# Performance work log

Hardware: AMD Instinct MI355X
Metric: run time of the kernel (lower is better)

## Reference

```python
import jax, jax.numpy as jnp
import numpy as np

B = 4096
NUM_FEATURES = 2048
NUM_NEURONS = 1024
NUM_TARGETS = 8
NNZ1 = 65536
NNZ2 = 8192


def _sparse_linear(x, w, b, rows, cols, n_out):
    """y[b, o] = sum_{e: rows[e]==o} w[e] * x[b, cols[e]] + b[o].

    x: [B, n_in], w: [nnz], rows/cols: [nnz] int, b: [n_out].
    """
    prod = x[:, cols] * w  # [B, nnz] gather + elementwise
    # segment_sum reduces over leading axis -> work on [nnz, B]
    y = jax.ops.segment_sum(prod.T, rows, num_segments=n_out)  # [n_out, B]
    return y.T + b


def setup_inputs() -> dict:
    key = jax.random.key(0)
    ks = jax.random.split(key, 9)
    x = jax.random.normal(ks[0], (B, NUM_FEATURES), dtype=jnp.float32)
    w1 = jax.random.normal(ks[1], (NNZ1,), dtype=jnp.float32) * 0.05
    b1 = jax.random.normal(ks[2], (NUM_NEURONS,), dtype=jnp.float32) * 0.05
    w2 = jax.random.normal(ks[3], (NNZ2,), dtype=jnp.float32) * 0.05
    b2 = jax.random.normal(ks[4], (NUM_TARGETS,), dtype=jnp.float32) * 0.05
    conn1_out = jax.random.randint(ks[5], (NNZ1,), 0, NUM_NEURONS, dtype=jnp.int64 if jax.config.jax_enable_x64 else jnp.int32)
    conn1_in = jax.random.randint(ks[6], (NNZ1,), 0, NUM_FEATURES, dtype=conn1_out.dtype)
    conn2_out = jax.random.randint(ks[7], (NNZ2,), 0, NUM_TARGETS, dtype=conn1_out.dtype)
    conn2_in = jax.random.randint(ks[8], (NNZ2,), 0, NUM_NEURONS, dtype=conn1_out.dtype)
    return {
        "x": x, "w1": w1, "b1": b1, "w2": w2, "b2": b2,
        "conn1_out": conn1_out, "conn1_in": conn1_in,
        "conn2_out": conn2_out, "conn2_in": conn2_in,
    }


def reference(x, w1, b1, w2, b2, conn1_out, conn1_in, conn2_out, conn2_in):
    h = jax.nn.sigmoid(_sparse_linear(x, w1, b1, conn1_out, conn1_in, b1.shape[0]))
    out = _sparse_linear(h, w2, b2, conn2_out, conn2_in, b2.shape[0])
    # num_targets = 8 != 1, so no final sigmoid (matches CrossEntropyLoss path)
    return out
```

## Files before the change

### kernel.cpp

```cpp
#include <hip/hip_runtime.h>
#include <math.h>

#define BATCH 4096
#define NFEAT 2048
#define NNEUR 1024
#define NTGT  8
#define NNZ1  65536
#define NNZ2  8192

#define BM 128
#define BN 64
#define BK 64
#define KSTEPS (NFEAT / BK)

typedef short  bf16x8 __attribute__((ext_vector_type(8)));
typedef float  f32x4  __attribute__((ext_vector_type(4)));

#define OFF_W1F  ((size_t)0)
#define OFF_W2D  ((size_t)8388608)
#define OFF_W1B  ((size_t)8421376)

#define ZERO_FLOAT4 526336
#define OUT_FLOAT4  (BATCH * NTGT / 4)

__device__ __forceinline__ unsigned short f2bf(float f) {
    union { float f; unsigned int u; } a; a.f = f;
    unsigned int u = a.u;
    u += 0x7fffu + ((u >> 16) & 1u);
    return (unsigned short)(u >> 16);
}

__device__ __forceinline__ uint4 pk8(float4 lo, float4 hi) {
    uint4 r;
    asm("v_cvt_pk_bf16_f32 %0, %1, %2" : "=v"(r.x) : "v"(lo.x), "v"(lo.y));
    asm("v_cvt_pk_bf16_f32 %0, %1, %2" : "=v"(r.y) : "v"(lo.z), "v"(lo.w));
    asm("v_cvt_pk_bf16_f32 %0, %1, %2" : "=v"(r.z) : "v"(hi.x), "v"(hi.y));
    asm("v_cvt_pk_bf16_f32 %0, %1, %2" : "=v"(r.w) : "v"(hi.z), "v"(hi.w));
    return r;
}

__global__ void k_zero(float4* __restrict__ ws4, float4* __restrict__ out4,
                       const float* __restrict__ b2) {
    int i = blockIdx.x * blockDim.x + threadIdx.x;
    if (i < ZERO_FLOAT4) {
        ws4[i] = make_float4(0.f, 0.f, 0.f, 0.f);
    } else {
        int j = i - ZERO_FLOAT4;
        if (j < OUT_FLOAT4) {
            int p = (j & 1) * 4;
            out4[j] = make_float4(b2[p], b2[p + 1], b2[p + 2], b2[p + 3]);
        }
    }
}

__global__ void k_build(const float* __restrict__ w1, const int* __restrict__ c1o,
                        const int* __restrict__ c1i,
                        const float* __restrict__ w2, const int* __restrict__ c2o,
                        const int* __restrict__ c2i,
                        float* __restrict__ W1f, float* __restrict__ W2d) {
    int i = blockIdx.x * blockDim.x + threadIdx.x;
    if (i < NNZ1) {
        atomicAdd(&W1f[(size_t)c1o[i] * NFEAT + c1i[i]], w1[i]);
    } else {
        int j = i - NNZ1;
        if (j < NNZ2) atomicAdd(&W2d[c2i[j] * NTGT + c2o[j]], w2[j]);
    }
}

__global__ void k_convert(const float* __restrict__ W1f, unsigned short* __restrict__ W1b) {
    int i = blockIdx.x * blockDim.x + threadIdx.x;
    float4 v = ((const float4*)W1f)[i];
    ushort4 o;
    o.x = f2bf(v.x); o.y = f2bf(v.y); o.z = f2bf(v.z); o.w = f2bf(v.w);
    ((ushort4*)W1b)[i] = o;
}

__global__ __launch_bounds__(256) void k_gemm(const unsigned short* __restrict__ W1b,
                                              const float* __restrict__ x,
                                              const float* __restrict__ b1,
                                              const float* __restrict__ W2d,
                                              float* __restrict__ out) {
    __shared__ unsigned short ldsA[2][BM * BK];
    __shared__ unsigned short ldsB[2][BN * BK];
    __shared__ float s_w2[BM][NTGT];
    __shared__ float s_b1[BM];
    __shared__ float s_pt[2][BN][NTGT];

    int bid = blockIdx.x;
    int v   = bid >> 3;
    int n0  = ((bid & 7) * 8 + (v >> 3)) * BN;
    int mt  = v & 7;
    int m0  = mt * BM;

    int tid  = threadIdx.x;
    int wv   = tid >> 6;
    int lane = tid & 63;
    int wm = wv >> 1, wn = wv & 1;
    int lr = lane & 15, lg = lane >> 4;

    for (int i = tid; i < BM * NTGT; i += 256)
        s_w2[i >> 3][i & 7] = W2d[(m0 + (i >> 3)) * NTGT + (i & 7)];
    if (tid < BM) s_b1[tid] = b1[m0 + tid];

    f32x4 zero4 = {0.f, 0.f, 0.f, 0.f};
    f32x4 acc[4][2];
#pragma unroll
    for (int i = 0; i < 4; ++i)
#pragma unroll
        for (int j = 0; j < 2; ++j) acc[i][j] = zero4;

    int r0 = tid >> 3, s0 = tid & 7;
    const unsigned short* gA0 = &W1b[(size_t)(m0 + r0) * NFEAT + s0 * 8];
    const unsigned short* gA1 = gA0 + 32 * NFEAT;
    const unsigned short* gA2 = gA0 + 64 * NFEAT;
    const unsigned short* gA3 = gA0 + 96 * NFEAT;
    const float* gB0 = &x[(size_t)(n0 + r0) * NFEAT + s0 * 8];
    const float* gB1 = gB0 + 32 * NFEAT;
    const int iw0 = r0 * 8 + (s0 ^ (r0 & 7));
    const int iw1 = iw0 + 256, iw2 = iw0 + 512, iw3 = iw0 + 768;

    bf16x8 A0a, A0b, A0c, A0d;  float4 B0a, B0b, B0c, B0d;
    bf16x8 A1a, A1b, A1c, A1d;  float4 B1a, B1b, B1c, B1d;
    bf16x8 af0[4], af1[4], bg0[2], bg1[2];

#define LOADS0(T) do { int kk = (T) * BK;                           \
        A0a = *(const bf16x8*)(gA0 + kk); A0b = *(const bf16x8*)(gA1 + kk); \
        A0c = *(const bf16x8*)(gA2 + kk); A0d = *(const bf16x8*)(gA3 + kk); \
        B0a = *(const float4*)(gB0 + kk); B0b = *(const float4*)(gB0 + kk + 4); \
        B0c = *(const float4*)(gB1 + kk); B0d = *(const float4*)(gB1 + kk + 4); } while (0)
#define LOADS1(T) do { int kk = (T) * BK;                           \
        A1a = *(const bf16x8*)(gA0 + kk); A1b = *(const bf16x8*)(gA1 + kk); \
        A1c = *(const bf16x8*)(gA2 + kk); A1d = *(const bf16x8*)(gA3 + kk); \
        B1a = *(const float4*)(gB0 + kk); B1b = *(const float4*)(gB0 + kk + 4); \
        B1c = *(const float4*)(gB1 + kk); B1d = *(const float4*)(gB1 + kk + 4); } while (0)

#define STORE0(BUF) do {                                            \
        bf16x8* dA = (bf16x8*)&ldsA[BUF][0];                        \
        dA[iw0] = A0a; dA[iw1] = A0b; dA[iw2] = A0c; dA[iw3] = A0d; \
        uint4* dB = (uint4*)&ldsB[BUF][0];                          \
        dB[iw0] = pk8(B0a, B0b); dB[iw1] = pk8(B0c, B0d); } while (0)
#define STORE1(BUF) do {                                            \
        bf16x8* dA = (bf16x8*)&ldsA[BUF][0];                        \
        dA[iw0] = A1a; dA[iw1] = A1b; dA[iw2] = A1c; dA[iw3] = A1d; \
        uint4* dB = (uint4*)&ldsB[BUF][0];                          \
        dB[iw0] = pk8(B1a, B1b); dB[iw1] = pk8(B1c, B1d); } while (0)

#define READF(BUF) do {                                             \
        const unsigned short* bA = ldsA[BUF];                       \
        const unsigned short* bB = ldsB[BUF];                       \
        _Pragma("unroll")                                           \
        for (int i = 0; i < 4; ++i) {                               \
            int rowa = wm * 64 + i * 16 + lr;                       \
            af0[i] = *(const bf16x8*)&bA[(rowa * 8 + ((lg)     ^ (rowa & 7))) * 8]; \
            af1[i] = *(const bf16x8*)&bA[(rowa * 8 + ((4 + lg) ^ (rowa & 7))) * 8]; \
        }                                                           \
        _Pragma("unroll")                                           \
        for (int j = 0; j < 2; ++j) {                               \
            int rowb = wn * 32 + j * 16 + lr;                       \
            bg0[j] = *(const bf16x8*)&bB[(rowb * 8 + ((lg)     ^ (rowb & 7))) * 8]; \
            bg1[j] = *(const bf16x8*)&bB[(rowb * 8 + ((4 + lg) ^ (rowb & 7))) * 8]; \
        }                                                           \
    } while (0)

#define MFMAS() do {                                                \
        _Pragma("unroll")                                           \
        for (int i = 0; i < 4; ++i)                                 \
            _Pragma("unroll")                                       \
            for (int j = 0; j < 2; ++j)                             \
                acc[i][j] = __builtin_amdgcn_mfma_f32_16x16x32_bf16(af0[i], bg0[j], acc[i][j], 0, 0, 0); \
        _Pragma("unroll")                                           \
        for (int i = 0; i < 4; ++i)                                 \
            _Pragma("unroll")                                       \
            for (int j = 0; j < 2; ++j)                             \
                acc[i][j] = __builtin_amdgcn_mfma_f32_16x16x32_bf16(af1[i], bg1[j], acc[i][j], 0, 0, 0); \
    } while (0)

#define LDSFENCE() asm volatile("s_waitcnt lgkmcnt(0)" ::: "memory")

    LOADS0(0);
    LOADS1(1);
    STORE0(0);
    LDSFENCE();
    __builtin_amdgcn_s_barrier();

#pragma unroll 1
    for (int p = 0; p < 15; ++p) {
        int e = 2 * p;
        LOADS0(e + 2);
        STORE1(1);
        READF(0);
        MFMAS();
        LDSFENCE();
        __builtin_amdgcn_s_barrier();
        LOADS1(e + 3);
        STORE0(0);
        READF(1);
        MFMAS();
        LDSFENCE();
        __builtin_amdgcn_s_barrier();
    }
    STORE1(1);
    READF(0);
    MFMAS();
    LDSFENCE();
    __builtin_amdgcn_s_barrier();
    READF(1);
    MFMAS();

#undef LOADS0
#undef LOADS1
#undef STORE0
#undef STORE1
#undef READF
#undef MFMAS
#undef LDSFENCE

    float pt[2][NTGT];
#pragma unroll
    for (int j = 0; j < 2; ++j)
#pragma unroll
        for (int t = 0; t < NTGT; ++t) pt[j][t] = 0.f;

#pragma unroll
    for (int i = 0; i < 4; ++i) {
#pragma unroll
        for (int r = 0; r < 4; ++r) {
            int ml = wm * 64 + i * 16 + lg * 4 + r;
            float bn = s_b1[ml];
#pragma unroll
            for (int j = 0; j < 2; ++j) {
                float h = 1.f / (1.f + __expf(-(acc[i][j][r] + bn)));
#pragma unroll
                for (int t = 0; t < NTGT; ++t)
                    pt[j][t] += h * s_w2[ml][t];
            }
        }
    }
#pragma unroll
    for (int j = 0; j < 2; ++j)
#pragma unroll
        for (int t = 0; t < NTGT; ++t) {
            float val = pt[j][t];
            val += __shfl_xor(val, 16, 64);
            val += __shfl_xor(val, 32, 64);
            pt[j][t] = val;
        }
    if (lg == 0) {
#pragma unroll
        for (int j = 0; j < 2; ++j) {
            int nl = wn * 32 + j * 16 + lr;
#pragma unroll
            for (int t = 0; t < NTGT; ++t)
                s_pt[wm][nl][t] = pt[j][t];
        }
    }
    __syncthreads();
    for (int idx = tid; idx < BN * NTGT; idx += 256) {
        int nl = idx >> 3, t = idx & 7;
        atomicAdd(&out[(size_t)(n0 + nl) * NTGT + t], s_pt[0][nl][t] + s_pt[1][nl][t]);
    }
}

extern "C" void kernel_launch(void* const* d_in, const int* in_sizes, int n_in,
                              void* d_out, int out_size, void* d_ws, size_t ws_size,
                              hipStream_t stream) {
    (void)in_sizes; (void)n_in; (void)out_size; (void)ws_size;
    const float* x   = (const float*)d_in[0];
    const float* w1  = (const float*)d_in[1];
    const float* b1  = (const float*)d_in[2];
    const float* w2  = (const float*)d_in[3];
    const float* b2  = (const float*)d_in[4];
    const int*   c1o = (const int*)d_in[5];
    const int*   c1i = (const int*)d_in[6];
    const int*   c2o = (const int*)d_in[7];
    const int*   c2i = (const int*)d_in[8];
    float* out = (float*)d_out;

    char* ws = (char*)d_ws;
    float*          W1f  = (float*)(ws + OFF_W1F);
    float*          W2d  = (float*)(ws + OFF_W2D);
    unsigned short* W1b  = (unsigned short*)(ws + OFF_W1B);

    k_zero<<<(ZERO_FLOAT4 + OUT_FLOAT4 + 255) / 256, 256, 0, stream>>>(
        (float4*)ws, (float4*)out, b2);

    k_build<<<(NNZ1 + NNZ2) / 256, 256, 0, stream>>>(w1, c1o, c1i, w2, c2o, c2i, W1f, W2d);

    k_convert<<<NNEUR * NFEAT / 4 / 256, 256, 0, stream>>>(W1f, W1b);

    k_gemm<<<(NNEUR / BM) * (BATCH / BN), 256, 0, stream>>>(W1b, x, b1, W2d, out);
}
```

Before: 50.41 us.

## Halve GEMM M-tile and split K across waves with LDS reduction

Shrinks the W1 row tile from 128 to 64, which doubles the number of GEMM blocks. Inside each block, the four waves are now split into two N-halves and two K-halves instead of an M×N grid. Each wave runs half the MFMAs per K-step, and the K-halves' accumulators are merged through LDS before the sigmoid/W2 epilogue. Launch bounds now request 4 blocks per SM for better occupancy and latency hiding. In exchange, the x tile is reloaded twice as often, an extra LDS round trip and barrier are added, and there are more output atomics.

Measured after the change: 59.08 us. 17.2% more time.

```diff
diff --git a/kernel.cpp b/kernel.cpp
--- a/kernel.cpp
+++ b/kernel.cpp
@@ -8,7 +8,7 @@
 #define NNZ1  65536
 #define NNZ2  8192
 
-#define BM 128
+#define BM 64
 #define BN 64
 #define BK 64
 #define KSTEPS (NFEAT / BK)
@@ -75,27 +75,27 @@
     ((ushort4*)W1b)[i] = o;
 }
 
-__global__ __launch_bounds__(256) void k_gemm(const unsigned short* __restrict__ W1b,
-                                              const float* __restrict__ x,
-                                              const float* __restrict__ b1,
-                                              const float* __restrict__ W2d,
-                                              float* __restrict__ out) {
+__global__ __launch_bounds__(256, 4) void k_gemm(const unsigned short* __restrict__ W1b,
+                                                 const float* __restrict__ x,
+                                                 const float* __restrict__ b1,
+                                                 const float* __restrict__ W2d,
+                                                 float* __restrict__ out) {
     __shared__ unsigned short ldsA[2][BM * BK];
     __shared__ unsigned short ldsB[2][BN * BK];
     __shared__ float s_w2[BM][NTGT];
     __shared__ float s_b1[BM];
-    __shared__ float s_pt[2][BN][NTGT];
+    __shared__ float s_pt[BN][NTGT];
 
     int bid = blockIdx.x;
     int v   = bid >> 3;
-    int n0  = ((bid & 7) * 8 + (v >> 3)) * BN;
-    int mt  = v & 7;
+    int n0  = ((bid & 7) * 8 + (v >> 4)) * BN;
+    int mt  = v & 15;
     int m0  = mt * BM;
 
     int tid  = threadIdx.x;
     int wv   = tid >> 6;
     int lane = tid & 63;
-    int wm = wv >> 1, wn = wv & 1;
+    int wn = wv >> 1, kh = wv & 1;
     int lr = lane & 15, lg = lane >> 4;
 
     for (int i = tid; i < BM * NTGT; i += 256)
@@ -112,36 +112,32 @@
     int r0 = tid >> 3, s0 = tid & 7;
     const unsigned short* gA0 = &W1b[(size_t)(m0 + r0) * NFEAT + s0 * 8];
     const unsigned short* gA1 = gA0 + 32 * NFEAT;
-    const unsigned short* gA2 = gA0 + 64 * NFEAT;
-    const unsigned short* gA3 = gA0 + 96 * NFEAT;
     const float* gB0 = &x[(size_t)(n0 + r0) * NFEAT + s0 * 8];
     const float* gB1 = gB0 + 32 * NFEAT;
     const int iw0 = r0 * 8 + (s0 ^ (r0 & 7));
-    const int iw1 = iw0 + 256, iw2 = iw0 + 512, iw3 = iw0 + 768;
-
-    bf16x8 A0a, A0b, A0c, A0d;  float4 B0a, B0b, B0c, B0d;
-    bf16x8 A1a, A1b, A1c, A1d;  float4 B1a, B1b, B1c, B1d;
-    bf16x8 af0[4], af1[4], bg0[2], bg1[2];
+    const int iw1 = iw0 + 256;
+
+    bf16x8 A0a, A0b;  float4 B0a, B0b, B0c, B0d;
+    bf16x8 A1a, A1b;  float4 B1a, B1b, B1c, B1d;
+    bf16x8 af[4], bg[2];
 
 #define LOADS0(T) do { int kk = (T) * BK;                           \
         A0a = *(const bf16x8*)(gA0 + kk); A0b = *(const bf16x8*)(gA1 + kk); \
-        A0c = *(const bf16x8*)(gA2 + kk); A0d = *(const bf16x8*)(gA3 + kk); \
         B0a = *(const float4*)(gB0 + kk); B0b = *(const float4*)(gB0 + kk + 4); \
         B0c = *(const float4*)(gB1 + kk); B0d = *(const float4*)(gB1 + kk + 4); } while (0)
 #define LOADS1(T) do { int kk = (T) * BK;                           \
         A1a = *(const bf16x8*)(gA0 + kk); A1b = *(const bf16x8*)(gA1 + kk); \
-        A1c = *(const bf16x8*)(gA2 + kk); A1d = *(const bf16x8*)(gA3 + kk); \
         B1a = *(const float4*)(gB0 + kk); B1b = *(const float4*)(gB0 + kk + 4); \
         B1c = *(const float4*)(gB1 + kk); B1d = *(const float4*)(gB1 + kk + 4); } while (0)
 
 #define STORE0(BUF) do {                                            \
         bf16x8* dA = (bf16x8*)&ldsA[BUF][0];                        \
-        dA[iw0] = A0a; dA[iw1] = A0b; dA[iw2] = A0c; dA[iw3] = A0d; \
+        dA[iw0] = A0a; dA[iw1] = A0b;                               \
         uint4* dB = (uint4*)&ldsB[BUF][0];                          \
         dB[iw0] = pk8(B0a, B0b); dB[iw1] = pk8(B0c, B0d); } while (0)
 #define STORE1(BUF) do {                                            \
         bf16x8* dA = (bf16x8*)&ldsA[BUF][0];                        \
-        dA[iw0] = A1a; dA[iw1] = A1b; dA[iw2] = A1c; dA[iw3] = A1d; \
+        dA[iw0] = A1a; dA[iw1] = A1b;                               \
         uint4* dB = (uint4*)&ldsB[BUF][0];                          \
         dB[iw0] = pk8(B1a, B1b); dB[iw1] = pk8(B1c, B1d); } while (0)
 
@@ -150,15 +146,13 @@
         const unsigned short* bB = ldsB[BUF];                       \
         _Pragma("unroll")                                           \
         for (int i = 0; i < 4; ++i) {                               \
-            int rowa = wm * 64 + i * 16 + lr;                       \
-            af0[i] = *(const bf16x8*)&bA[(rowa * 8 + ((lg)     ^ (rowa & 7))) * 8]; \
-            af1[i] = *(const bf16x8*)&bA[(rowa * 8 + ((4 + lg) ^ (rowa & 7))) * 8]; \
+            int rowa = i * 16 + lr;                                 \
+            af[i] = *(const bf16x8*)&bA[(rowa * 8 + ((kh * 4 + lg) ^ (rowa & 7))) * 8]; \
         }                                                           \
         _Pragma("unroll")                                           \
         for (int j = 0; j < 2; ++j) {                               \
             int rowb = wn * 32 + j * 16 + lr;                       \
-            bg0[j] = *(const bf16x8*)&bB[(rowb * 8 + ((lg)     ^ (rowb & 7))) * 8]; \
-            bg1[j] = *(const bf16x8*)&bB[(rowb * 8 + ((4 + lg) ^ (rowb & 7))) * 8]; \
+            bg[j] = *(const bf16x8*)&bB[(rowb * 8 + ((kh * 4 + lg) ^ (rowb & 7))) * 8]; \
         }                                                           \
     } while (0)
 
@@ -167,12 +161,7 @@
         for (int i = 0; i < 4; ++i)                                 \
             _Pragma("unroll")                                       \
             for (int j = 0; j < 2; ++j)                             \
-                acc[i][j] = __builtin_amdgcn_mfma_f32_16x16x32_bf16(af0[i], bg0[j], acc[i][j], 0, 0, 0); \
-        _Pragma("unroll")                                           \
-        for (int i = 0; i < 4; ++i)                                 \
-            _Pragma("unroll")                                       \
-            for (int j = 0; j < 2; ++j)                             \
-                acc[i][j] = __builtin_amdgcn_mfma_f32_16x16x32_bf16(af1[i], bg1[j], acc[i][j], 0, 0, 0); \
+                acc[i][j] = __builtin_amdgcn_mfma_f32_16x16x32_bf16(af[i], bg[j], acc[i][j], 0, 0, 0); \
     } while (0)
 
 #define LDSFENCE() asm volatile("s_waitcnt lgkmcnt(0)" ::: "memory")
@@ -213,51 +202,73 @@
 #undef STORE1
 #undef READF
 #undef MFMAS
-#undef LDSFENCE
-
-    float pt[2][NTGT];
-#pragma unroll
-    for (int j = 0; j < 2; ++j)
-#pragma unroll
-        for (int t = 0; t < NTGT; ++t) pt[j][t] = 0.f;
-
-#pragma unroll
-    for (int i = 0; i < 4; ++i) {
-#pragma unroll
-        for (int r = 0; r < 4; ++r) {
-            int ml = wm * 64 + i * 16 + lg * 4 + r;
-            float bn = s_b1[ml];
+
+    LDSFENCE();
+    __builtin_amdgcn_s_barrier();
+    float* cmb = (float*)&ldsA[0][0];
+    if (kh == 1) {
+#pragma unroll
+        for (int i = 0; i < 4; ++i)
+#pragma unroll
+            for (int j = 0; j < 2; ++j)
+                *(f32x4*)&cmb[wn * 2048 + (i * 2 + j) * 256 + lane * 4] = acc[i][j];
+    }
+    LDSFENCE();
+    __builtin_amdgcn_s_barrier();
+
+    if (kh == 0) {
+#pragma unroll
+        for (int i = 0; i < 4; ++i)
 #pragma unroll
             for (int j = 0; j < 2; ++j) {
-                float h = 1.f / (1.f + __expf(-(acc[i][j][r] + bn)));
-#pragma unroll
-                for (int t = 0; t < NTGT; ++t)
-                    pt[j][t] += h * s_w2[ml][t];
+                f32x4 o = *(const f32x4*)&cmb[wn * 2048 + (i * 2 + j) * 256 + lane * 4];
+                acc[i][j] += o;
+            }
+
+        float pt[2][NTGT];
+#pragma unroll
+        for (int j = 0; j < 2; ++j)
+#pragma unroll
+            for (int t = 0; t < NTGT; ++t) pt[j][t] = 0.f;
+
+#pragma unroll
+        for (int i = 0; i < 4; ++i) {
+#pragma unroll
+            for (int r = 0; r < 4; ++r) {
+                int ml = i * 16 + lg * 4 + r;
+                float bn = s_b1[ml];
+#pragma unroll
+                for (int j = 0; j < 2; ++j) {
+                    float h = 1.f / (1.f + __expf(-(acc[i][j][r] + bn)));
+#pragma unroll
+                    for (int t = 0; t < NTGT; ++t)
+                        pt[j][t] += h * s_w2[ml][t];
+                }
             }
         }
-    }
-#pragma unroll
-    for (int j = 0; j < 2; ++j)
-#pragma unroll
-        for (int t = 0; t < NTGT; ++t) {
-            float val = pt[j][t];
-            val += __shfl_xor(val, 16, 64);
-            val += __shfl_xor(val, 32, 64);
-            pt[j][t] = val;
-        }
-    if (lg == 0) {
-#pragma unroll
-        for (int j = 0; j < 2; ++j) {
-            int nl = wn * 32 + j * 16 + lr;
-#pragma unroll
-            for (int t = 0; t < NTGT; ++t)
-                s_pt[wm][nl][t] = pt[j][t];
+#pragma unroll
+        for (int j = 0; j < 2; ++j)
+#pragma unroll
+            for (int t = 0; t < NTGT; ++t) {
+                float val = pt[j][t];
+                val += __shfl_xor(val, 16, 64);
+                val += __shfl_xor(val, 32, 64);
+                pt[j][t] = val;
+            }
+        if (lg == 0) {
+#pragma unroll
+            for (int j = 0; j < 2; ++j) {
+                int nl = wn * 32 + j * 16 + lr;
+#pragma unroll
+                for (int t = 0; t < NTGT; ++t)
+                    s_pt[nl][t] = pt[j][t];
+            }
         }
     }
     __syncthreads();
     for (int idx = tid; idx < BN * NTGT; idx += 256) {
         int nl = idx >> 3, t = idx & 7;
-        atomicAdd(&out[(size_t)(n0 + nl) * NTGT + t], s_pt[0][nl][t] + s_pt[1][nl][t]);
+        atomicAdd(&out[(size_t)(n0 + nl) * NTGT + t], s_pt[nl][t]);
     }
 }
 
```

## Enlarge GEMM tile to 128x128 with 32x32x16 MFMA and shallower K step

Applied to the files above, without the earlier changes.

Widens the batch tile from 64 to 128 columns and halves the K step to 32. It also replaces the 16x16x32 bf16 MFMAs with 32x32x16 ones, using a new XOR swizzle for the narrower LDS rows and an updated epilogue row mapping. The aim is more reuse of each loaded W1 and x tile, fewer global loads per FLOP, and fewer, larger matrix instructions. The trade-offs are half as many blocks to fill the GPU, more barriers because there are twice as many K iterations, and more accumulator registers per lane. The launch grid must shrink to match, and that code is not visible here.

Result: slower. 56.79 us (+12.7%).

```diff
diff --git a/kernel.cpp b/kernel.cpp
--- a/kernel.cpp
+++ b/kernel.cpp
@@ -9,12 +9,12 @@
 #define NNZ2  8192
 
 #define BM 128
-#define BN 64
-#define BK 64
+#define BN 128
+#define BK 32
 #define KSTEPS (NFEAT / BK)
 
 typedef short  bf16x8 __attribute__((ext_vector_type(8)));
-typedef float  f32x4  __attribute__((ext_vector_type(4)));
+typedef float  f32x16 __attribute__((ext_vector_type(16)));
 
 #define OFF_W1F  ((size_t)0)
 #define OFF_W2D  ((size_t)8388608)
@@ -88,7 +88,7 @@
 
     int bid = blockIdx.x;
     int v   = bid >> 3;
-    int n0  = ((bid & 7) * 8 + (v >> 3)) * BN;
+    int n0  = ((bid & 7) * 4 + (v >> 3)) * BN;
     int mt  = v & 7;
     int m0  = mt * BM;
 
@@ -96,52 +96,48 @@
     int wv   = tid >> 6;
     int lane = tid & 63;
     int wm = wv >> 1, wn = wv & 1;
-    int lr = lane & 15, lg = lane >> 4;
+    int lc = lane & 31;
+    int lh = lane >> 5;
 
     for (int i = tid; i < BM * NTGT; i += 256)
         s_w2[i >> 3][i & 7] = W2d[(m0 + (i >> 3)) * NTGT + (i & 7)];
     if (tid < BM) s_b1[tid] = b1[m0 + tid];
 
-    f32x4 zero4 = {0.f, 0.f, 0.f, 0.f};
-    f32x4 acc[4][2];
-#pragma unroll
-    for (int i = 0; i < 4; ++i)
-#pragma unroll
-        for (int j = 0; j < 2; ++j) acc[i][j] = zero4;
-
-    int r0 = tid >> 3, s0 = tid & 7;
+    f32x16 acc[2][2];
+#pragma unroll
+    for (int i = 0; i < 2; ++i)
+#pragma unroll
+        for (int j = 0; j < 2; ++j) acc[i][j] = (f32x16)(0.f);
+
+    int r0 = tid >> 2, s0 = tid & 3;
     const unsigned short* gA0 = &W1b[(size_t)(m0 + r0) * NFEAT + s0 * 8];
-    const unsigned short* gA1 = gA0 + 32 * NFEAT;
-    const unsigned short* gA2 = gA0 + 64 * NFEAT;
-    const unsigned short* gA3 = gA0 + 96 * NFEAT;
+    const unsigned short* gA1 = gA0 + (size_t)64 * NFEAT;
     const float* gB0 = &x[(size_t)(n0 + r0) * NFEAT + s0 * 8];
-    const float* gB1 = gB0 + 32 * NFEAT;
-    const int iw0 = r0 * 8 + (s0 ^ (r0 & 7));
-    const int iw1 = iw0 + 256, iw2 = iw0 + 512, iw3 = iw0 + 768;
-
-    bf16x8 A0a, A0b, A0c, A0d;  float4 B0a, B0b, B0c, B0d;
-    bf16x8 A1a, A1b, A1c, A1d;  float4 B1a, B1b, B1c, B1d;
-    bf16x8 af0[4], af1[4], bg0[2], bg1[2];
+    const float* gB1 = gB0 + (size_t)64 * NFEAT;
+    const int iw0 = r0 * 4 + (s0 ^ (r0 & 3) ^ ((r0 >> 2) & 3));
+    const int iw1 = iw0 + 256;
+
+    bf16x8 A0a, A0b;  float4 B0a, B0b, B0c, B0d;
+    bf16x8 A1a, A1b;  float4 B1a, B1b, B1c, B1d;
+    bf16x8 af[2][2], bg[2][2];
 
 #define LOADS0(T) do { int kk = (T) * BK;                           \
         A0a = *(const bf16x8*)(gA0 + kk); A0b = *(const bf16x8*)(gA1 + kk); \
-        A0c = *(const bf16x8*)(gA2 + kk); A0d = *(const bf16x8*)(gA3 + kk); \
         B0a = *(const float4*)(gB0 + kk); B0b = *(const float4*)(gB0 + kk + 4); \
         B0c = *(const float4*)(gB1 + kk); B0d = *(const float4*)(gB1 + kk + 4); } while (0)
 #define LOADS1(T) do { int kk = (T) * BK;                           \
         A1a = *(const bf16x8*)(gA0 + kk); A1b = *(const bf16x8*)(gA1 + kk); \
-        A1c = *(const bf16x8*)(gA2 + kk); A1d = *(const bf16x8*)(gA3 + kk); \
         B1a = *(const float4*)(gB0 + kk); B1b = *(const float4*)(gB0 + kk + 4); \
         B1c = *(const float4*)(gB1 + kk); B1d = *(const float4*)(gB1 + kk + 4); } while (0)
 
 #define STORE0(BUF) do {                                            \
         bf16x8* dA = (bf16x8*)&ldsA[BUF][0];                        \
-        dA[iw0] = A0a; dA[iw1] = A0b; dA[iw2] = A0c; dA[iw3] = A0d; \
+        dA[iw0] = A0a; dA[iw1] = A0b;                               \
         uint4* dB = (uint4*)&ldsB[BUF][0];                          \
         dB[iw0] = pk8(B0a, B0b); dB[iw1] = pk8(B0c, B0d); } while (0)
 #define STORE1(BUF) do {                                            \
         bf16x8* dA = (bf16x8*)&ldsA[BUF][0];                        \
-        dA[iw0] = A1a; dA[iw1] = A1b; dA[iw2] = A1c; dA[iw3] = A1d; \
+        dA[iw0] = A1a; dA[iw1] = A1b;                               \
         uint4* dB = (uint4*)&ldsB[BUF][0];                          \
         dB[iw0] = pk8(B1a, B1b); dB[iw1] = pk8(B1c, B1d); } while (0)
 
@@ -149,30 +145,26 @@
         const unsigned short* bA = ldsA[BUF];                       \
         const unsigned short* bB = ldsB[BUF];                       \
         _Pragma("unroll")                                           \
-        for (int i = 0; i < 4; ++i) {                               \
-            int rowa = wm * 64 + i * 16 + lr;                       \
-            af0[i] = *(const bf16x8*)&bA[(rowa * 8 + ((lg)     ^ (rowa & 7))) * 8]; \
-            af1[i] = *(const bf16x8*)&bA[(rowa * 8 + ((4 + lg) ^ (rowa & 7))) * 8]; \
-        }                                                           \
-        _Pragma("unroll")                                           \
-        for (int j = 0; j < 2; ++j) {                               \
-            int rowb = wn * 32 + j * 16 + lr;                       \
-            bg0[j] = *(const bf16x8*)&bB[(rowb * 8 + ((lg)     ^ (rowb & 7))) * 8]; \
-            bg1[j] = *(const bf16x8*)&bB[(rowb * 8 + ((4 + lg) ^ (rowb & 7))) * 8]; \
+        for (int f = 0; f < 2; ++f) {                               \
+            int ra = wm * 64 + f * 32 + lc;                         \
+            int xa = (ra & 3) ^ ((ra >> 2) & 3);                    \
+            af[f][0] = *(const bf16x8*)&bA[(ra * 4 + ((lh)     ^ xa)) * 8]; \
+            af[f][1] = *(const bf16x8*)&bA[(ra * 4 + ((2 + lh) ^ xa)) * 8]; \
+            int rb = wn * 64 + f * 32 + lc;                         \
+            int xb2 = (rb & 3) ^ ((rb >> 2) & 3);                   \
+            bg[f][0] = *(const bf16x8*)&bB[(rb * 4 + ((lh)     ^ xb2)) * 8]; \
+            bg[f][1] = *(const bf16x8*)&bB[(rb * 4 + ((2 + lh) ^ xb2)) * 8]; \
         }                                                           \
     } while (0)
 
 #define MFMAS() do {                                                \
         _Pragma("unroll")                                           \
-        for (int i = 0; i < 4; ++i)                                 \
+        for (int kk = 0; kk < 2; ++kk)                              \
             _Pragma("unroll")                                       \
-            for (int j = 0; j < 2; ++j)                             \
-                acc[i][j] = __builtin_amdgcn_mfma_f32_16x16x32_bf16(af0[i], bg0[j], acc[i][j], 0, 0, 0); \
-        _Pragma("unroll")                                           \
-        for (int i = 0; i < 4; ++i)                                 \
-            _Pragma("unroll")                                       \
-            for (int j = 0; j < 2; ++j)                             \
-                acc[i][j] = __builtin_amdgcn_mfma_f32_16x16x32_bf16(af1[i], bg1[j], acc[i][j], 0, 0, 0); \
+            for (int i = 0; i < 2; ++i)                             \
+                _Pragma("unroll")                                   \
+                for (int j = 0; j < 2; ++j)                         \
+                    acc[i][j] = __builtin_amdgcn_mfma_f32_32x32x16_bf16(af[i][kk], bg[j][kk], acc[i][j], 0, 0, 0); \
     } while (0)
 
 #define LDSFENCE() asm volatile("s_waitcnt lgkmcnt(0)" ::: "memory")
@@ -184,7 +176,7 @@
     __builtin_amdgcn_s_barrier();
 
 #pragma unroll 1
-    for (int p = 0; p < 15; ++p) {
+    for (int p = 0; p < KSTEPS / 2 - 1; ++p) {
         int e = 2 * p;
         LOADS0(e + 2);
         STORE1(1);
@@ -213,7 +205,6 @@
 #undef STORE1
 #undef READF
 #undef MFMAS
-#undef LDSFENCE
 
     float pt[2][NTGT];
 #pragma unroll
@@ -222,10 +213,10 @@
         for (int t = 0; t < NTGT; ++t) pt[j][t] = 0.f;
 
 #pragma unroll
-    for (int i = 0; i < 4; ++i) {
-#pragma unroll
-        for (int r = 0; r < 4; ++r) {
-            int ml = wm * 64 + i * 16 + lg * 4 + r;
+    for (int i = 0; i < 2; ++i) {
+#pragma unroll
+        for (int r = 0; r < 16; ++r) {
+            int ml = wm * 64 + i * 32 + (r & 3) + 8 * (r >> 2) + 4 * lh;
             float bn = s_b1[ml];
 #pragma unroll
             for (int j = 0; j < 2; ++j) {
@@ -239,16 +230,12 @@
 #pragma unroll
     for (int j = 0; j < 2; ++j)
 #pragma unroll
-        for (int t = 0; t < NTGT; ++t) {
-            float val = pt[j][t];
-            val += __shfl_xor(val, 16, 64);
-            val += __shfl_xor(val, 32, 64);
-            pt[j][t] = val;
-        }
-    if (lg == 0) {
+        for (int t = 0; t < NTGT; ++t)
+            pt[j][t] += __shfl_xor(pt[j][t], 32, 64);
+    if (lh == 0) {
 #pragma unroll
         for (int j = 0; j < 2; ++j) {
-            int nl = wn * 32 + j * 16 + lr;
+            int nl = wn * 64 + j * 32 + lc;
 #pragma unroll
             for (int t = 0; t < NTGT; ++t)
                 s_pt[wm][nl][t] = pt[j][t];
```

## Pre-pack W1 into MFMA fragment layout and load A directly to registers

Applied to the files above, without the earlier changes.

Replaces the bf16 conversion kernel with a pack kernel that writes W1 already arranged in per-lane MFMA fragment order. The GEMM then loads A fragments straight from global memory into registers, with no LDS staging or reads for A, which cuts LDS traffic and frees LDS. Block-to-tile mapping is also changed to group M/N tiles per XCD for better L2 reuse. The cost is more registers for the double-buffered A fragments and redundant global A loads across the two wn waves.

New measurement: 52.59 us. 4.3% more time.

```diff
diff --git a/kernel.cpp b/kernel.cpp
--- a/kernel.cpp
+++ b/kernel.cpp
@@ -18,17 +18,10 @@
 
 #define OFF_W1F  ((size_t)0)
 #define OFF_W2D  ((size_t)8388608)
-#define OFF_W1B  ((size_t)8421376)
+#define OFF_W1P  ((size_t)8421376)
 
 #define ZERO_FLOAT4 526336
 #define OUT_FLOAT4  (BATCH * NTGT / 4)
-
-__device__ __forceinline__ unsigned short f2bf(float f) {
-    union { float f; unsigned int u; } a; a.f = f;
-    unsigned int u = a.u;
-    u += 0x7fffu + ((u >> 16) & 1u);
-    return (unsigned short)(u >> 16);
-}
 
 __device__ __forceinline__ uint4 pk8(float4 lo, float4 hi) {
     uint4 r;
@@ -67,30 +60,36 @@
     }
 }
 
-__global__ void k_convert(const float* __restrict__ W1f, unsigned short* __restrict__ W1b) {
-    int i = blockIdx.x * blockDim.x + threadIdx.x;
-    float4 v = ((const float4*)W1f)[i];
-    ushort4 o;
-    o.x = f2bf(v.x); o.y = f2bf(v.y); o.z = f2bf(v.z); o.w = f2bf(v.w);
-    ((ushort4*)W1b)[i] = o;
-}
-
-__global__ __launch_bounds__(256) void k_gemm(const unsigned short* __restrict__ W1b,
+__global__ void k_pack(const float* __restrict__ W1f, unsigned short* __restrict__ W1p) {
+    int u = blockIdx.x * blockDim.x + threadIdx.x;
+    int lane  = u & 63;
+    int kslot = (u >> 6) & 1;
+    int i     = (u >> 7) & 3;
+    int ks    = (u >> 9) & 31;
+    int mt    = u >> 14;
+    int row = mt * 64 + i * 16 + (lane & 15);
+    int k   = ks * 64 + kslot * 32 + (lane >> 4) * 8;
+    const float* src = &W1f[(size_t)row * NFEAT + k];
+    float4 lo = *(const float4*)src;
+    float4 hi = *(const float4*)(src + 4);
+    ((uint4*)W1p)[u] = pk8(lo, hi);
+}
+
+__global__ __launch_bounds__(256) void k_gemm(const unsigned short* __restrict__ W1p,
                                               const float* __restrict__ x,
                                               const float* __restrict__ b1,
                                               const float* __restrict__ W2d,
                                               float* __restrict__ out) {
-    __shared__ unsigned short ldsA[2][BM * BK];
     __shared__ unsigned short ldsB[2][BN * BK];
     __shared__ float s_w2[BM][NTGT];
     __shared__ float s_b1[BM];
     __shared__ float s_pt[2][BN][NTGT];
 
     int bid = blockIdx.x;
-    int v   = bid >> 3;
-    int n0  = ((bid & 7) * 8 + (v >> 3)) * BN;
-    int mt  = v & 7;
-    int m0  = mt * BM;
+    int xcd = bid & 7;
+    int loc = bid >> 3;
+    int m0  = ((xcd & 1) * 4 + (loc & 3)) * BM;
+    int n0  = ((xcd >> 1) * 16 + (loc >> 2)) * BN;
 
     int tid  = threadIdx.x;
     int wv   = tid >> 6;
@@ -109,51 +108,42 @@
 #pragma unroll
         for (int j = 0; j < 2; ++j) acc[i][j] = zero4;
 
+    int mtA = (m0 >> 6) + wm;
+    const bf16x8* gAf = (const bf16x8*)W1p + (size_t)mtA * 16384 + lane;
+
     int r0 = tid >> 3, s0 = tid & 7;
-    const unsigned short* gA0 = &W1b[(size_t)(m0 + r0) * NFEAT + s0 * 8];
-    const unsigned short* gA1 = gA0 + 32 * NFEAT;
-    const unsigned short* gA2 = gA0 + 64 * NFEAT;
-    const unsigned short* gA3 = gA0 + 96 * NFEAT;
     const float* gB0 = &x[(size_t)(n0 + r0) * NFEAT + s0 * 8];
     const float* gB1 = gB0 + 32 * NFEAT;
     const int iw0 = r0 * 8 + (s0 ^ (r0 & 7));
-    const int iw1 = iw0 + 256, iw2 = iw0 + 512, iw3 = iw0 + 768;
-
-    bf16x8 A0a, A0b, A0c, A0d;  float4 B0a, B0b, B0c, B0d;
-    bf16x8 A1a, A1b, A1c, A1d;  float4 B1a, B1b, B1c, B1d;
-    bf16x8 af0[4], af1[4], bg0[2], bg1[2];
-
-#define LOADS0(T) do { int kk = (T) * BK;                           \
-        A0a = *(const bf16x8*)(gA0 + kk); A0b = *(const bf16x8*)(gA1 + kk); \
-        A0c = *(const bf16x8*)(gA2 + kk); A0d = *(const bf16x8*)(gA3 + kk); \
+    const int iw1 = iw0 + 256;
+
+    bf16x8 Af0[8], Af1[8];
+    float4 B0a, B0b, B0c, B0d;
+    float4 B1a, B1b, B1c, B1d;
+    bf16x8 bg0[2], bg1[2];
+
+#define LOADSA0(T) do {                                             \
+        _Pragma("unroll")                                           \
+        for (int c = 0; c < 8; ++c) Af0[c] = gAf[(T) * 512 + c * 64]; } while (0)
+#define LOADSA1(T) do {                                             \
+        _Pragma("unroll")                                           \
+        for (int c = 0; c < 8; ++c) Af1[c] = gAf[(T) * 512 + c * 64]; } while (0)
+#define LOADSB0(T) do { int kk = (T) * BK;                          \
         B0a = *(const float4*)(gB0 + kk); B0b = *(const float4*)(gB0 + kk + 4); \
         B0c = *(const float4*)(gB1 + kk); B0d = *(const float4*)(gB1 + kk + 4); } while (0)
-#define LOADS1(T) do { int kk = (T) * BK;                           \
-        A1a = *(const bf16x8*)(gA0 + kk); A1b = *(const bf16x8*)(gA1 + kk); \
-        A1c = *(const bf16x8*)(gA2 + kk); A1d = *(const bf16x8*)(gA3 + kk); \
+#define LOADSB1(T) do { int kk = (T) * BK;                          \
         B1a = *(const float4*)(gB0 + kk); B1b = *(const float4*)(gB0 + kk + 4); \
         B1c = *(const float4*)(gB1 + kk); B1d = *(const float4*)(gB1 + kk + 4); } while (0)
 
 #define STORE0(BUF) do {                                            \
-        bf16x8* dA = (bf16x8*)&ldsA[BUF][0];                        \
-        dA[iw0] = A0a; dA[iw1] = A0b; dA[iw2] = A0c; dA[iw3] = A0d; \
         uint4* dB = (uint4*)&ldsB[BUF][0];                          \
         dB[iw0] = pk8(B0a, B0b); dB[iw1] = pk8(B0c, B0d); } while (0)
 #define STORE1(BUF) do {                                            \
-        bf16x8* dA = (bf16x8*)&ldsA[BUF][0];                        \
-        dA[iw0] = A1a; dA[iw1] = A1b; dA[iw2] = A1c; dA[iw3] = A1d; \
         uint4* dB = (uint4*)&ldsB[BUF][0];                          \
         dB[iw0] = pk8(B1a, B1b); dB[iw1] = pk8(B1c, B1d); } while (0)
 
 #define READF(BUF) do {                                             \
-        const unsigned short* bA = ldsA[BUF];                       \
         const unsigned short* bB = ldsB[BUF];                       \
-        _Pragma("unroll")                                           \
-        for (int i = 0; i < 4; ++i) {                               \
-            int rowa = wm * 64 + i * 16 + lr;                       \
-            af0[i] = *(const bf16x8*)&bA[(rowa * 8 + ((lg)     ^ (rowa & 7))) * 8]; \
-            af1[i] = *(const bf16x8*)&bA[(rowa * 8 + ((4 + lg) ^ (rowa & 7))) * 8]; \
-        }                                                           \
         _Pragma("unroll")                                           \
         for (int j = 0; j < 2; ++j) {                               \
             int rowb = wn * 32 + j * 16 + lr;                       \
@@ -162,23 +152,37 @@
         }                                                           \
     } while (0)
 
-#define MFMAS() do {                                                \
+#define MFMAS0() do {                                               \
         _Pragma("unroll")                                           \
         for (int i = 0; i < 4; ++i)                                 \
             _Pragma("unroll")                                       \
             for (int j = 0; j < 2; ++j)                             \
-                acc[i][j] = __builtin_amdgcn_mfma_f32_16x16x32_bf16(af0[i], bg0[j], acc[i][j], 0, 0, 0); \
+                acc[i][j] = __builtin_amdgcn_mfma_f32_16x16x32_bf16(Af0[i * 2],     bg0[j], acc[i][j], 0, 0, 0); \
         _Pragma("unroll")                                           \
         for (int i = 0; i < 4; ++i)                                 \
             _Pragma("unroll")                                       \
             for (int j = 0; j < 2; ++j)                             \
-                acc[i][j] = __builtin_amdgcn_mfma_f32_16x16x32_bf16(af1[i], bg1[j], acc[i][j], 0, 0, 0); \
+                acc[i][j] = __builtin_amdgcn_mfma_f32_16x16x32_bf16(Af0[i * 2 + 1], bg1[j], acc[i][j], 0, 0, 0); \
     } while (0)
+#define MFMAS1() do {                                               \
+        _Pragma("unroll")                                           \
+        for (int i = 0; i < 4; ++i)                                 \
+            _Pragma("unroll")                                       \
+            for (int j = 0; j < 2; ++j)                             \
+                acc[i][j] = __builtin_amdgcn_mfma_f32_16x16x32_bf16(Af1[i * 2],     bg0[j], acc[i][j], 0, 0, 0); \
+        _Pragma("unroll")                                           \
+        for (int i = 0; i < 4; ++i)                                 \
+            _Pragma("unroll")                                       \
+            for (int j = 0; j < 2; ++j)                             \
+                acc[i][j] = __builtin_amdgcn_mfma_f32_16x16x32_bf16(Af1[i * 2 + 1], bg1[j], acc[i][j], 0, 0, 0); \
+    } while (0)
 
 #define LDSFENCE() asm volatile("s_waitcnt lgkmcnt(0)" ::: "memory")
 
-    LOADS0(0);
-    LOADS1(1);
+    LOADSB0(0);
+    LOADSA0(0);
+    LOADSB1(1);
+    LOADSA1(1);
     STORE0(0);
     LDSFENCE();
     __builtin_amdgcn_s_barrier();
@@ -186,33 +190,38 @@
 #pragma unroll 1
     for (int p = 0; p < 15; ++p) {
         int e = 2 * p;
-        LOADS0(e + 2);
+        LOADSB0(e + 2);
         STORE1(1);
         READF(0);
-        MFMAS();
+        MFMAS0();
+        LOADSA0(e + 2);
         LDSFENCE();
         __builtin_amdgcn_s_barrier();
-        LOADS1(e + 3);
+        LOADSB1(e + 3);
         STORE0(0);
         READF(1);
-        MFMAS();
+        MFMAS1();
+        LOADSA1(e + 3);
         LDSFENCE();
         __builtin_amdgcn_s_barrier();
     }
     STORE1(1);
     READF(0);
-    MFMAS();
+    MFMAS0();
     LDSFENCE();
     __builtin_amdgcn_s_barrier();
     READF(1);
-    MFMAS();
-
-#undef LOADS0
-#undef LOADS1
+    MFMAS1();
+
+#undef LOADSA0
+#undef LOADSA1
+#undef LOADSB0
+#undef LOADSB1
 #undef STORE0
 #undef STORE1
 #undef READF
-#undef MFMAS
+#undef MFMAS0
+#undef MFMAS1
 #undef LDSFENCE
 
     float pt[2][NTGT];
@@ -279,14 +288,14 @@
     char* ws = (char*)d_ws;
     float*          W1f  = (float*)(ws + OFF_W1F);
     float*          W2d  = (float*)(ws + OFF_W2D);
-    unsigned short* W1b  = (unsigned short*)(ws + OFF_W1B);
+    unsigned short* W1p  = (unsigned short*)(ws + OFF_W1P);
 
     k_zero<<<(ZERO_FLOAT4 + OUT_FLOAT4 + 255) / 256, 256, 0, stream>>>(
         (float4*)ws, (float4*)out, b2);
 
     k_build<<<(NNZ1 + NNZ2) / 256, 256, 0, stream>>>(w1, c1o, c1i, w2, c2o, c2i, W1f, W2d);
 
-    k_convert<<<NNEUR * NFEAT / 4 / 256, 256, 0, stream>>>(W1f, W1b);
-
-    k_gemm<<<(NNEUR / BM) * (BATCH / BN), 256, 0, stream>>>(W1b, x, b1, W2d, out);
-}
+    k_pack<<<NNEUR * NFEAT / 8 / 256, 256, 0, stream>>>(W1f, W1p);
+
+    k_gemm<<<(NNEUR / BM) * (BATCH / BN), 256, 0, stream>>>(W1p, x, b1, W2d, out);
+}
```
